# Kernel optimization log

Hardware: AMD Instinct MI355X
Metric: run time of the kernel (lower is better)

Reference implementation:

```python
import jax, jax.numpy as jnp
import numpy as np

B, S, D_DEC, D_ENC, F, U = 64, 8192, 128, 128, 16, 128
CLIP_C = 10.0
BIG_NUMBER = 1e9


def setup_inputs() -> dict:
    key = jax.random.key(0)
    ks = jax.random.split(key, 10)
    scale = 1.0 / np.sqrt(U)
    return {
        "dec_output": jax.random.normal(ks[0], (B, 1, D_DEC), dtype=jnp.float32),
        "enc_input": jax.random.normal(ks[1], (B, S, F), dtype=jnp.float32),
        "enc_outputs": jax.random.normal(ks[2], (B, S, D_ENC), dtype=jnp.float32),
        "mask": jax.random.bernoulli(ks[3], 0.3, (B, S)).astype(jnp.float32),
        "W1_w": jax.random.uniform(ks[4], (D_DEC, U), jnp.float32, -scale, scale),
        "W1_b": jnp.zeros((U,), jnp.float32),
        "W2_w": jax.random.uniform(ks[5], (D_ENC, U), jnp.float32, -scale, scale),
        "W2_b": jnp.zeros((U,), jnp.float32),
        "V_w": jax.random.uniform(ks[6], (U, 1), jnp.float32, -scale, scale),
        "V_b": jnp.zeros((1,), jnp.float32),
    }


def reference(dec_output, enc_input, enc_outputs, mask, W1_w, W1_b, W2_w, W2_b, V_w, V_b):
    # dec_output: [B,1,Ddec] (already has time dim; add_time_dim=False)
    q = dec_output @ W1_w + W1_b                  # [B,1,U]
    k = enc_outputs @ W2_w + W2_b                 # [B,S,U]
    score = jnp.tanh(q + k) @ V_w + V_b           # [B,S,1]
    pointer_logits = jnp.squeeze(score, axis=2)   # [B,S]
    pointer_logits = CLIP_C * jnp.tanh(pointer_logits)
    pointer_logits = pointer_logits - mask * BIG_NUMBER
    pointer_probs = jax.nn.softmax(pointer_logits, axis=-1)
    pointer_index = jnp.argmax(pointer_probs, axis=-1).astype(jnp.int32)  # [B]
    gathered = enc_input[jnp.arange(enc_input.shape[0]), pointer_index]   # [B,F]
    return (pointer_logits, pointer_probs, pointer_index, gathered)
```

## Files before the change

### kernel.cpp

```cpp
#include <hip/hip_runtime.h>
#include <cmath>

constexpr int Bn   = 64;
constexpr int Sn   = 8192;
constexpr int DDEC = 128;
constexpr int DENC = 128;
constexpr int Fn   = 16;
constexpr int Un   = 128;

using bf16x8 = __attribute__((ext_vector_type(8))) short;
using f32x4  = __attribute__((ext_vector_type(4))) float;

__device__ __forceinline__ float fast_tanh(float x) {
    float ax = fabsf(x);
    float e  = __expf(2.0f * ax);
    float t  = 1.0f - 2.0f * __builtin_amdgcn_rcpf(e + 1.0f);
    return copysignf(t, x);
}

__device__ __forceinline__ unsigned int fkey(float f) {
    unsigned int u = __float_as_uint(f);
    return (u & 0x80000000u) ? ~u : (u | 0x80000000u);
}

__device__ __forceinline__ unsigned int bf16_rne(float f) {
    unsigned int u = __float_as_uint(f);
    return (u + 0x7FFFu + ((u >> 16) & 1u)) >> 16;
}

__global__ void setup_kernel(const float* __restrict__ dec,
                             const float* __restrict__ W1,
                             const float* __restrict__ W1b,
                             const float* __restrict__ W2,
                             const float* __restrict__ W2b,
                             float* __restrict__ qq,
                             uint4* __restrict__ wftab,
                             float* __restrict__ sums,
                             unsigned long long* __restrict__ amax) {
    int blk = blockIdx.x, tid = threadIdx.x;
    if (blk < Bn) {
        if (tid < Un) {
            int b = blk, u = tid;
            float acc = W1b[u] + W2b[u];
            #pragma unroll 8
            for (int d = 0; d < DDEC; ++d)
                acc = fmaf(dec[b * DDEC + d], W1[d * Un + u], acc);
            qq[b * Un + u] = acc;
        }
        if (tid == 0) { sums[blk] = 0.0f; amax[blk] = 0ull; }
    } else {
        int n = blk - Bn;
        int c = tid >> 6;
        int lane = tid & 63;
        int d0 = c * 32 + (lane >> 4) * 8;
        int u  = n * 16 + (lane & 15);
        unsigned int r[8];
        #pragma unroll
        for (int t = 0; t < 8; ++t)
            r[t] = bf16_rne(W2[(d0 + t) * Un + u]);
        uint4 out;
        out.x = r[0] | (r[1] << 16);
        out.y = r[2] | (r[3] << 16);
        out.z = r[4] | (r[5] << 16);
        out.w = r[6] | (r[7] << 16);
        wftab[(n * 4 + c) * 64 + lane] = out;
    }
}

__device__ __forceinline__ void cvt_hilo(float4 a, float4 b, uint4& hi, uint4& lo) {
    unsigned int ua[8] = { __float_as_uint(a.x), __float_as_uint(a.y),
                           __float_as_uint(a.z), __float_as_uint(a.w),
                           __float_as_uint(b.x), __float_as_uint(b.y),
                           __float_as_uint(b.z), __float_as_uint(b.w) };
    float fa[8] = { a.x, a.y, a.z, a.w, b.x, b.y, b.z, b.w };
    unsigned int vl[8];
    #pragma unroll
    for (int j = 0; j < 8; ++j) {
        float hf = __uint_as_float(ua[j] & 0xFFFF0000u);
        vl[j] = __float_as_uint(fa[j] - hf);
    }
    hi.x = (ua[1] & 0xFFFF0000u) | (ua[0] >> 16);
    hi.y = (ua[3] & 0xFFFF0000u) | (ua[2] >> 16);
    hi.z = (ua[5] & 0xFFFF0000u) | (ua[4] >> 16);
    hi.w = (ua[7] & 0xFFFF0000u) | (ua[6] >> 16);
    lo.x = (vl[1] & 0xFFFF0000u) | (vl[0] >> 16);
    lo.y = (vl[3] & 0xFFFF0000u) | (vl[2] >> 16);
    lo.z = (vl[5] & 0xFFFF0000u) | (vl[4] >> 16);
    lo.w = (vl[7] & 0xFFFF0000u) | (vl[6] >> 16);
}

__global__ __launch_bounds__(256, 2)
void score_kernel(const float* __restrict__ enc,
                  const float* __restrict__ mask,
                  const float* __restrict__ qq,
                  const uint4* __restrict__ wftab,
                  const float* __restrict__ V,
                  const float* __restrict__ Vb,
                  float* __restrict__ logits,
                  float* __restrict__ probs,
                  float* __restrict__ sums,
                  unsigned long long* __restrict__ amax) {
    const int tid  = threadIdx.x;
    const int lane = tid & 63;
    const int wv   = tid >> 6;
    const int wave_id = blockIdx.x * 4 + wv;
    const int base = wave_id * 256;
    const int b    = base >> 13;
    const int g    = lane >> 4;
    const int li   = lane & 15;

    uint4 wf[32];
    #pragma unroll
    for (int i = 0; i < 32; ++i) wf[i] = wftab[i * 64 + lane];

    float qv[8], Vl[8];
    #pragma unroll
    for (int n = 0; n < 8; ++n) {
        qv[n] = qq[b * Un + n * 16 + li];
        Vl[n] = V[n * 16 + li];
    }
    const float Vbias = Vb[0];
    const bool active = (li < 4);

    const float4* eptr = (const float4*)enc;
    float4 ebuf[8];
    {
        size_t i0 = (size_t)(base + li) * 32 + g * 2;
        #pragma unroll
        for (int c = 0; c < 4; ++c) {
            ebuf[2 * c]     = eptr[i0 + c * 8];
            ebuf[2 * c + 1] = eptr[i0 + c * 8 + 1];
        }
    }

    float psum = 0.0f;
    unsigned long long key = 0ull;

    #pragma unroll 1
    for (int st = 0; st < 16; ++st) {
        const int myrow = base + st * 16 + 4 * g + li;
        float mval = 0.0f;
        if (active) mval = mask[myrow];

        f32x4 acc[8];
        #pragma unroll
        for (int n = 0; n < 8; ++n)
            acc[n] = f32x4{qv[n], qv[n], qv[n], qv[n]};

        #pragma unroll
        for (int c = 0; c < 4; ++c) {
            uint4 hi, lo;
            cvt_hilo(ebuf[2 * c], ebuf[2 * c + 1], hi, lo);
            bf16x8 ah = __builtin_bit_cast(bf16x8, hi);
            bf16x8 al = __builtin_bit_cast(bf16x8, lo);
            #pragma unroll
            for (int n = 0; n < 8; ++n)
                acc[n] = __builtin_amdgcn_mfma_f32_16x16x32_bf16(
                    ah, __builtin_bit_cast(bf16x8, wf[n * 4 + c]), acc[n], 0, 0, 0);
            #pragma unroll
            for (int n = 0; n < 8; ++n)
                acc[n] = __builtin_amdgcn_mfma_f32_16x16x32_bf16(
                    al, __builtin_bit_cast(bf16x8, wf[n * 4 + c]), acc[n], 0, 0, 0);
        }

        if (st < 15) {
            size_t i0 = (size_t)(base + (st + 1) * 16 + li) * 32 + g * 2;
            #pragma unroll
            for (int c = 0; c < 4; ++c) {
                ebuf[2 * c]     = eptr[i0 + c * 8];
                ebuf[2 * c + 1] = eptr[i0 + c * 8 + 1];
            }
        }

        float pr0 = 0.0f, pr1 = 0.0f, pr2 = 0.0f, pr3 = 0.0f;
        #pragma unroll
        for (int n = 0; n < 8; ++n) {
            pr0 = fmaf(fast_tanh(acc[n][0]), Vl[n], pr0);
            pr1 = fmaf(fast_tanh(acc[n][1]), Vl[n], pr1);
            pr2 = fmaf(fast_tanh(acc[n][2]), Vl[n], pr2);
            pr3 = fmaf(fast_tanh(acc[n][3]), Vl[n], pr3);
        }
        #pragma unroll
        for (int off = 1; off < 16; off <<= 1) {
            pr0 += __shfl_xor(pr0, off);
            pr1 += __shfl_xor(pr1, off);
            pr2 += __shfl_xor(pr2, off);
            pr3 += __shfl_xor(pr3, off);
        }
        if (active) {
            float sc = (li == 0) ? pr0 : (li == 1) ? pr1 : (li == 2) ? pr2 : pr3;
            sc += Vbias;
            float l = 10.0f * fast_tanh(sc) - mval * 1e9f;
            logits[myrow] = l;
            float p = __expf(l - 10.0f);
            probs[myrow] = p;
            psum += p;
            unsigned long long k =
                ((unsigned long long)fkey(l) << 32) |
                (unsigned int)(Sn - 1 - (myrow & (Sn - 1)));
            if (k > key) key = k;
        }
    }

    #pragma unroll
    for (int off = 1; off < 64; off <<= 1) {
        psum += __shfl_xor(psum, off);
        unsigned long long ok = __shfl_xor(key, off);
        if (ok > key) key = ok;
    }
    if (lane == 0) {
        atomicAdd(&sums[b], psum);
        atomicMax(&amax[b], key);
    }
}

__global__ __launch_bounds__(256)
void argfix_kernel(const float* __restrict__ logits,
                   const float* __restrict__ enc,
                   const float* __restrict__ qq,
                   const float* __restrict__ W2,
                   const float* __restrict__ V,
                   const float* __restrict__ Vb,
                   const float* __restrict__ enc_in,
                   const unsigned long long* __restrict__ amax,
                   float* __restrict__ out_idx,
                   float* __restrict__ out_gath) {
    int b = blockIdx.x, tid = threadIdx.x;
    __shared__ int cnt;
    __shared__ int cand[64];
    __shared__ float red[256];
    __shared__ float bestL;
    __shared__ int bestI;
    if (tid == 0) { cnt = 0; bestL = -INFINITY; bestI = 0x7fffffff; }
    __syncthreads();

    unsigned int hk = (unsigned int)(amax[b] >> 32);
    float M = (hk & 0x80000000u) ? __uint_as_float(hk & 0x7FFFFFFFu)
                                 : __uint_as_float(~hk);
    const float* lrow = logits + (size_t)b * Sn;
    for (int s = tid; s < Sn; s += 256) {
        if (lrow[s] >= M - 0.125f) {
            int i = atomicAdd(&cnt, 1);
            if (i < 64) cand[i] = s;
        }
    }
    __syncthreads();
    int n = min(cnt, 64);
    int u = tid & 127, h = tid >> 7;

    for (int c = 0; c < n; ++c) {
        int row_s = cand[c];
        const float* erow = enc + ((size_t)b * Sn + row_s) * DENC;
        float kp = 0.0f;
        #pragma unroll 8
        for (int dd = 0; dd < 64; ++dd) {
            int d = h * 64 + dd;
            kp = fmaf(erow[d], W2[d * Un + u], kp);
        }
        red[tid] = kp;
        __syncthreads();
        if (tid < 128) {
            float kk = red[tid] + red[tid + 128] + qq[b * Un + tid];
            red[tid] = fast_tanh(kk) * V[tid];
        }
        __syncthreads();
        for (int off = 64; off > 0; off >>= 1) {
            if (tid < off) red[tid] += red[tid + off];
            __syncthreads();
        }
        if (tid == 0) {
            float sc = red[0] + Vb[0];
            float l = 10.0f * fast_tanh(sc);
            if (l > bestL || (l == bestL && row_s < bestI)) { bestL = l; bestI = row_s; }
        }
        __syncthreads();
    }

    if (tid == 0) out_idx[b] = (float)bestI;
    __syncthreads();
    if (tid < Fn) out_gath[b * Fn + tid] = enc_in[((size_t)b * Sn + bestI) * Fn + tid];
}

__global__ __launch_bounds__(256)
void finalize_kernel(const float* __restrict__ sums,
                     float* __restrict__ probs) {
    int row = blockIdx.x * 256 + threadIdx.x;
    int b = row >> 13;
    probs[row] *= 1.0f / sums[b];
}

extern "C" void kernel_launch(void* const* d_in, const int* in_sizes, int n_in,
                              void* d_out, int out_size, void* d_ws, size_t ws_size,
                              hipStream_t stream) {
    const float* dec    = (const float*)d_in[0];
    const float* enc_in = (const float*)d_in[1];
    const float* enc    = (const float*)d_in[2];
    const float* mask   = (const float*)d_in[3];
    const float* W1     = (const float*)d_in[4];
    const float* W1b    = (const float*)d_in[5];
    const float* W2     = (const float*)d_in[6];
    const float* W2b    = (const float*)d_in[7];
    const float* V      = (const float*)d_in[8];
    const float* Vb     = (const float*)d_in[9];

    float* qq   = (float*)d_ws;
    float* sums = qq + Bn * Un;
    unsigned long long* amax =
        (unsigned long long*)(sums + Bn);
    uint4* wftab = (uint4*)(amax + Bn);

    float* logits = (float*)d_out;
    float* probs  = logits + (size_t)Bn * Sn;
    float* oidx   = probs + (size_t)Bn * Sn;
    float* ogath  = oidx + Bn;

    setup_kernel<<<Bn + 8, 256, 0, stream>>>(dec, W1, W1b, W2, W2b, qq, wftab, sums, amax);
    score_kernel<<<(Bn * Sn) / (256 * 4), 256, 0, stream>>>(
        enc, mask, qq, wftab, V, Vb, logits, probs, sums, amax);
    argfix_kernel<<<Bn, 256, 0, stream>>>(
        logits, enc, qq, W2, V, Vb, enc_in, amax, oidx, ogath);
    finalize_kernel<<<(Bn * Sn) / 256, 256, 0, stream>>>(sums, probs);
}
```

Baseline: 442.5 us.

## Merge argfix and finalize kernels, vectorize normalization, hoist prefetch before MFMAs

Folds the argmax-fix kernel and the probability-normalization kernel into one launch: the first blocks scale probs by the inverse row sum using float4 loads, and the trailing blocks do the per-batch argmax refinement and gather. In the score kernel, the bf16 hi/lo conversion of the current tile is done up front so the next tile's global loads can be issued before the MFMA chain, which gives more overlap between memory and compute. This saves one kernel launch and cuts the number of normalization threads by four. The cost is more live registers in the score loop for the converted fragments plus the extra prefetch buffer.

```diff
diff --git a/kernel.cpp b/kernel.cpp
--- a/kernel.cpp
+++ b/kernel.cpp
@@ -142,17 +142,28 @@
         float mval = 0.0f;
         if (active) mval = mask[myrow];
 
+        uint4 fh[4], fl[4];
+        #pragma unroll
+        for (int c = 0; c < 4; ++c)
+            cvt_hilo(ebuf[2 * c], ebuf[2 * c + 1], fh[c], fl[c]);
+
+        if (st < 15) {
+            size_t i0 = (size_t)(base + (st + 1) * 16 + li) * 32 + g * 2;
+            #pragma unroll
+            for (int c = 0; c < 4; ++c) {
+                ebuf[2 * c]     = eptr[i0 + c * 8];
+                ebuf[2 * c + 1] = eptr[i0 + c * 8 + 1];
+            }
+        }
+
         f32x4 acc[8];
         #pragma unroll
         for (int n = 0; n < 8; ++n)
             acc[n] = f32x4{qv[n], qv[n], qv[n], qv[n]};
-
         #pragma unroll
         for (int c = 0; c < 4; ++c) {
-            uint4 hi, lo;
-            cvt_hilo(ebuf[2 * c], ebuf[2 * c + 1], hi, lo);
-            bf16x8 ah = __builtin_bit_cast(bf16x8, hi);
-            bf16x8 al = __builtin_bit_cast(bf16x8, lo);
+            bf16x8 ah = __builtin_bit_cast(bf16x8, fh[c]);
+            bf16x8 al = __builtin_bit_cast(bf16x8, fl[c]);
             #pragma unroll
             for (int n = 0; n < 8; ++n)
                 acc[n] = __builtin_amdgcn_mfma_f32_16x16x32_bf16(
@@ -161,15 +172,6 @@
             for (int n = 0; n < 8; ++n)
                 acc[n] = __builtin_amdgcn_mfma_f32_16x16x32_bf16(
                     al, __builtin_bit_cast(bf16x8, wf[n * 4 + c]), acc[n], 0, 0, 0);
-        }
-
-        if (st < 15) {
-            size_t i0 = (size_t)(base + (st + 1) * 16 + li) * 32 + g * 2;
-            #pragma unroll
-            for (int c = 0; c < 4; ++c) {
-                ebuf[2 * c]     = eptr[i0 + c * 8];
-                ebuf[2 * c + 1] = eptr[i0 + c * 8 + 1];
-            }
         }
 
         float pr0 = 0.0f, pr1 = 0.0f, pr2 = 0.0f, pr3 = 0.0f;
@@ -215,17 +217,32 @@
 }
 
 __global__ __launch_bounds__(256)
-void argfix_kernel(const float* __restrict__ logits,
-                   const float* __restrict__ enc,
-                   const float* __restrict__ qq,
-                   const float* __restrict__ W2,
-                   const float* __restrict__ V,
-                   const float* __restrict__ Vb,
-                   const float* __restrict__ enc_in,
-                   const unsigned long long* __restrict__ amax,
-                   float* __restrict__ out_idx,
-                   float* __restrict__ out_gath) {
-    int b = blockIdx.x, tid = threadIdx.x;
+void finalize_kernel(const float* __restrict__ logits,
+                     const float* __restrict__ enc,
+                     const float* __restrict__ qq,
+                     const float* __restrict__ W2,
+                     const float* __restrict__ V,
+                     const float* __restrict__ Vb,
+                     const float* __restrict__ enc_in,
+                     const float* __restrict__ sums,
+                     const unsigned long long* __restrict__ amax,
+                     float* __restrict__ probs,
+                     float* __restrict__ out_idx,
+                     float* __restrict__ out_gath) {
+    int blk = blockIdx.x;
+    int tid = threadIdx.x;
+    if (blk < (Bn * Sn) / (256 * 4)) {
+        int i4 = blk * 256 + tid;
+        int b = i4 >> 11;
+        float inv = 1.0f / sums[b];
+        float4* p4 = (float4*)probs;
+        float4 v = p4[i4];
+        v.x *= inv; v.y *= inv; v.z *= inv; v.w *= inv;
+        p4[i4] = v;
+        return;
+    }
+    int b = blk - (Bn * Sn) / (256 * 4);
+
     __shared__ int cnt;
     __shared__ int cand[64];
     __shared__ float red[256];
@@ -279,14 +296,6 @@
     if (tid == 0) out_idx[b] = (float)bestI;
     __syncthreads();
     if (tid < Fn) out_gath[b * Fn + tid] = enc_in[((size_t)b * Sn + bestI) * Fn + tid];
-}
-
-__global__ __launch_bounds__(256)
-void finalize_kernel(const float* __restrict__ sums,
-                     float* __restrict__ probs) {
-    int row = blockIdx.x * 256 + threadIdx.x;
-    int b = row >> 13;
-    probs[row] *= 1.0f / sums[b];
 }
 
 extern "C" void kernel_launch(void* const* d_in, const int* in_sizes, int n_in,
@@ -317,7 +326,6 @@
     setup_kernel<<<Bn + 8, 256, 0, stream>>>(dec, W1, W1b, W2, W2b, qq, wftab, sums, amax);
     score_kernel<<<(Bn * Sn) / (256 * 4), 256, 0, stream>>>(
         enc, mask, qq, wftab, V, Vb, logits, probs, sums, amax);
-    argfix_kernel<<<Bn, 256, 0, stream>>>(
-        logits, enc, qq, W2, V, Vb, enc_in, amax, oidx, ogath);
-    finalize_kernel<<<(Bn * Sn) / 256, 256, 0, stream>>>(sums, probs);
-}
+    finalize_kernel<<<(Bn * Sn) / (256 * 4) + Bn, 256, 0, stream>>>(
+        logits, enc, qq, W2, V, Vb, enc_in, sums, amax, probs, oidx, ogath);
+}
```

Result: no change. 439.3 us (-0.7%).
